# Kernel tuning notes

Measured on AMD Instinct MI355X. Metric: run time of the kernel, lower is better.

Reference implementation:

```python
import jax, jax.numpy as jnp
import numpy as np

H = 8          # num_heads
EPS = 1e-6     # layernorm epsilon
NEG_INF = -1e9


def _ln(x, g, b):
    m = jnp.mean(x, axis=-1, keepdims=True)
    v = jnp.mean(jnp.square(x - m), axis=-1, keepdims=True)
    return g * (x - m) * jax.lax.rsqrt(v + EPS) + b


def _mha(xq, kv, wq, wk, wv, wo, bias):
    # xq: [B,Tq,D], kv: [B,Tk,D]; weights [D,D]. Returns (out [B,Tq,D], weights [B,H,Tq,Tk]).
    B, Tq, D = xq.shape
    dh = D // H
    q = (xq @ wq) * (dh ** -0.5)
    k = kv @ wk
    v = kv @ wv
    q = q.reshape(B, Tq, H, dh).transpose(0, 2, 1, 3)
    k = k.reshape(B, -1, H, dh).transpose(0, 2, 1, 3)
    v = v.reshape(B, -1, H, dh).transpose(0, 2, 1, 3)
    logits = jnp.einsum('bhqd,bhkd->bhqk', q, k)
    if bias is not None:
        logits = logits + bias
    w = jax.nn.softmax(logits, axis=-1)
    out = jnp.einsum('bhqk,bhkd->bhqd', w, v).transpose(0, 2, 1, 3).reshape(B, Tq, D)
    return out @ wo, w


def setup_inputs() -> dict:
    key = jax.random.key(0)
    ks = jax.random.split(key, 16)
    B, Td, Te, D, F, L = 2, 2048, 2048, 512, 2048, 2
    s = 0.02
    inp = {
        'x': jax.random.normal(ks[0], (B, Td, D), jnp.float32),
        'enc_a': jax.random.normal(ks[1], (B, Te, D), jnp.float32),
        'enc_c': jax.random.normal(ks[2], (B, Te, D), jnp.float32),
        'sa_wq': jax.random.normal(ks[3], (L, D, D), jnp.float32) * s,
        'sa_wk': jax.random.normal(ks[4], (L, D, D), jnp.float32) * s,
        'sa_wv': jax.random.normal(ks[5], (L, D, D), jnp.float32) * s,
        'sa_wo': jax.random.normal(ks[6], (L, D, D), jnp.float32) * s,
        'ed_wq': jax.random.normal(ks[7], (L, D, D), jnp.float32) * s,
        'ed_wk': jax.random.normal(ks[8], (L, D, D), jnp.float32) * s,
        'ed_wv': jax.random.normal(ks[9], (L, D, D), jnp.float32) * s,
        'ed_wo': jax.random.normal(ks[10], (L, D, D), jnp.float32) * s,
        'ffn_w1': jax.random.normal(ks[11], (L, D, F), jnp.float32) * s,
        'ffn_w2': jax.random.normal(ks[12], (L, F, D), jnp.float32) * s,
        'ln1_g': jnp.ones((L, D), jnp.float32), 'ln1_b': jnp.zeros((L, D), jnp.float32),
        'ln2_g': jnp.ones((L, D), jnp.float32), 'ln2_b': jnp.zeros((L, D), jnp.float32),
        'ln3_g': jnp.ones((L, D), jnp.float32), 'ln3_b': jnp.zeros((L, D), jnp.float32),
        'out_g': jnp.ones((D,), jnp.float32), 'out_b': jnp.zeros((D,), jnp.float32),
    }
    return inp


def reference(x, enc_a, enc_c, sa_wq, sa_wk, sa_wv, sa_wo, ed_wq, ed_wk, ed_wv, ed_wo,
              ffn_w1, ffn_w2, ln1_g, ln1_b, ln2_g, ln2_b, ln3_g, ln3_b, out_g, out_b):
    B, T, D = x.shape
    L = sa_wq.shape[0]
    # decoder self-attention causal bias, broadcast over [B,H]
    causal = jnp.where(jnp.tril(jnp.ones((T, T), bool)), 0.0, NEG_INF)[None, None]
    avg = None
    for i in range(L):
        h = _ln(x, ln1_g[i], ln1_b[i])
        y, _ = _mha(h, h, sa_wq[i], sa_wk[i], sa_wv[i], sa_wo[i], causal)
        x = x + y  # residual (dropout inactive at eval)
        h = _ln(x, ln2_g[i], ln2_b[i])
        y0, _ = _mha(h, enc_a, ed_wq[i], ed_wk[i], ed_wv[i], ed_wo[i], None)
        y1, w = _mha(h, enc_c, ed_wq[i], ed_wk[i], ed_wv[i], ed_wo[i], None)
        # original overwrites attn_scores with second call's head-averaged weights
        scores = jnp.mean(w, axis=1) / L
        avg = scores if avg is None else avg + scores
        x = x + y0 + y1
        h = _ln(x, ln3_g[i], ln3_b[i])
        x = x + jax.nn.relu(h @ ffn_w1[i]) @ ffn_w2[i]
    x = _ln(x, out_g, out_b)
    return x, avg
```

## Files before the change

### kernel.cpp

```cpp
#include <hip/hip_runtime.h>
#include <hip/hip_bf16.h>

#define BB 2
#define TT 2048
#define DD 512
#define FF 2048
#define HH 8
#define DH 64
#define LL 2
#define MM (BB*TT)

typedef __attribute__((ext_vector_type(8))) short bf16x8;
typedef __attribute__((ext_vector_type(4))) float f32x4;

__device__ __forceinline__ float bf2f(unsigned short u) {
    return __uint_as_float(((unsigned int)u) << 16);
}
__device__ __forceinline__ unsigned short f2bf(float f) {
    unsigned int u = __float_as_uint(f);
    u += 0x7fffu + ((u >> 16) & 1u);
    return (unsigned short)(u >> 16);
}
__device__ __forceinline__ void gload16(const void* g, void* l) {
    __builtin_amdgcn_global_load_lds((__attribute__((address_space(1))) void*)g,
                                     (__attribute__((address_space(3))) void*)l, 16, 0, 0);
}

template<bool BF16OUT>
__global__ __launch_bounds__(256) void ln_kernel(const float* __restrict__ x,
                                                 const float* __restrict__ g,
                                                 const float* __restrict__ b,
                                                 void* __restrict__ out)
{
    const int row = blockIdx.x;
    const int tid = threadIdx.x;
    const float2 v = ((const float2*)(x + (size_t)row * DD))[tid];
    float s = v.x + v.y;
    float q = v.x * v.x + v.y * v.y;
    #pragma unroll
    for (int off = 32; off; off >>= 1) {
        s += __shfl_down(s, off);
        q += __shfl_down(q, off);
    }
    __shared__ float ss[4], qq[4];
    const int wid = tid >> 6;
    if ((tid & 63) == 0) { ss[wid] = s; qq[wid] = q; }
    __syncthreads();
    s = ss[0] + ss[1] + ss[2] + ss[3];
    q = qq[0] + qq[1] + qq[2] + qq[3];
    const float mean = s * (1.0f / DD);
    const float var = q * (1.0f / DD) - mean * mean;
    const float inv = rsqrtf(var + 1e-6f);
    const float2 gg = ((const float2*)g)[tid];
    const float2 bb = ((const float2*)b)[tid];
    const float ox = gg.x * (v.x - mean) * inv + bb.x;
    const float oy = gg.y * (v.y - mean) * inv + bb.y;
    if (BF16OUT) {
        const unsigned int pk = (unsigned int)f2bf(ox) | ((unsigned int)f2bf(oy) << 16);
        ((unsigned int*)((unsigned short*)out + (size_t)row * DD))[tid] = pk;
    } else {
        float2 o; o.x = ox; o.y = oy;
        ((float2*)((float*)out + (size_t)row * DD))[tid] = o;
    }
}

__global__ __launch_bounds__(256) void cvt_kernel(const float* __restrict__ src,
                                                  unsigned short* __restrict__ dst, int n)
{
    const int i = (blockIdx.x * 256 + threadIdx.x) * 8;
    if (i >= n) return;
    const float4 a = *(const float4*)(src + i);
    const float4 b = *(const float4*)(src + i + 4);
    unsigned short o[8];
    o[0] = f2bf(a.x); o[1] = f2bf(a.y); o[2] = f2bf(a.z); o[3] = f2bf(a.w);
    o[4] = f2bf(b.x); o[5] = f2bf(b.y); o[6] = f2bf(b.z); o[7] = f2bf(b.w);
    *(bf16x8*)(dst + i) = *(bf16x8*)o;
}

struct CvtJob { const float* s; unsigned short* d; };
struct CvtJobs16 { CvtJob j[16]; };

__global__ __launch_bounds__(256) void cvtT_kernel(CvtJobs16 P, int K, int N)
{
    __shared__ float t[32][33];
    const CvtJob jb = P.j[blockIdx.z];
    const int tx = threadIdx.x & 31, ty = threadIdx.x >> 5;
    const int gk = blockIdx.y << 5, gn = blockIdx.x << 5;
    #pragma unroll
    for (int i = 0; i < 4; ++i)
        t[ty + i * 8][tx] = jb.s[(size_t)(gk + ty + i * 8) * N + gn + tx];
    __syncthreads();
    #pragma unroll
    for (int i = 0; i < 4; ++i)
        jb.d[(size_t)(gn + ty + i * 8) * K + gk + tx] = f2bf(t[tx][ty + i * 8]);
}

__global__ __launch_bounds__(256) void vtrans_kernel(const unsigned short* __restrict__ v,
                                                     unsigned short* __restrict__ vt)
{
    __shared__ unsigned short tile[64][72];
    const int b = blockIdx.z, h = blockIdx.y, t0 = blockIdx.x << 6;
    const int r = threadIdx.x >> 2;
    const int s4 = threadIdx.x & 3;
    const unsigned short* src = v + (size_t)(b * TT + t0 + r) * DD + h * DH + s4 * 16;
    *(bf16x8*)&tile[r][s4 * 16] = *(const bf16x8*)src;
    *(bf16x8*)&tile[r][s4 * 16 + 8] = *(const bf16x8*)(src + 8);
    __syncthreads();
    unsigned short o[16];
    #pragma unroll
    for (int e = 0; e < 16; ++e) o[e] = tile[s4 * 16 + e][r];
    unsigned short* dst = vt + ((size_t)(b * HH + h) * DH + r) * TT + t0 + s4 * 16;
    *(bf16x8*)dst = *(bf16x8*)o;
    *(bf16x8*)(dst + 8) = *(bf16x8*)(o + 8);
}

struct GemmJob {
    const unsigned short* A;
    const unsigned short* Wt;
    const float* res;
    float* Cf;
    unsigned short* Cb;
    float scale;
    int relu;
};
struct GemmJobs6 { GemmJob j[6]; };

__global__ __launch_bounds__(256, 2) void gemm_mfma(GemmJobs6 P, int M, int N, int K)
{
    __shared__ __align__(16) unsigned char lds[32768];
    const GemmJob jb = P.j[blockIdx.z];
    const int tid = threadIdx.x, lane = tid & 63, w = tid >> 6;
    const int bn = blockIdx.x << 7, bm = blockIdx.y << 7;
    const int wr = (w >> 1) << 6, wc = (w & 1) << 6;
    const size_t strA = (size_t)K * 2;

    f32x4 acc[4][4] = {};
    const int akey = (lane & 7) << 4;
    const int frow = lane & 15;
    const int kq = (lane >> 4) << 4;

    for (int kt = 0; kt < K; kt += 64) {
        __syncthreads();
        #pragma unroll
        for (int c = 0; c < 4; ++c) {
            const int q = c * 4 + w;
            const int o = (q << 10) + (lane << 4);
            const int row = o >> 7;
            const int colb = (o & 127) ^ ((row & 7) << 4);
            gload16((const char*)jb.A + (size_t)(bm + row) * strA + kt * 2 + colb,
                    lds + (q << 10));
            gload16((const char*)jb.Wt + (size_t)(bn + row) * strA + kt * 2 + colb,
                    lds + 16384 + (q << 10));
        }
        asm volatile("s_waitcnt vmcnt(0)" ::: "memory");
        __syncthreads();
        #pragma unroll
        for (int kk = 0; kk < 2; ++kk) {
            bf16x8 av[4], bv[4];
            #pragma unroll
            for (int i = 0; i < 4; ++i) {
                const int rA = wr + (i << 4) + frow;
                av[i] = *(const bf16x8*)(lds + (rA << 7) + ((((kk << 6) + kq)) ^ akey));
                const int rB = wc + (i << 4) + frow;
                bv[i] = *(const bf16x8*)(lds + 16384 + (rB << 7) + ((((kk << 6) + kq)) ^ akey));
            }
            #pragma unroll
            for (int i = 0; i < 4; ++i)
                #pragma unroll
                for (int j = 0; j < 4; ++j)
                    acc[i][j] = __builtin_amdgcn_mfma_f32_16x16x32_bf16(av[i], bv[j], acc[i][j], 0, 0, 0);
        }
    }

    const int crow0 = (lane >> 4) << 2;
    const int ccol = lane & 15;
    #pragma unroll
    for (int i = 0; i < 4; ++i) {
        #pragma unroll
        for (int j = 0; j < 4; ++j) {
            #pragma unroll
            for (int r = 0; r < 4; ++r) {
                const int gm = bm + wr + (i << 4) + crow0 + r;
                const int gn = bn + wc + (j << 4) + ccol;
                float v = acc[i][j][r] * jb.scale;
                if (jb.relu) v = fmaxf(v, 0.f);
                const size_t idx = (size_t)gm * N + gn;
                if (jb.res) v += jb.res[idx];
                if (jb.Cf) jb.Cf[idx] = v;
                if (jb.Cb) jb.Cb[idx] = f2bf(v);
            }
        }
    }
}

template<bool CAUSAL, bool DUAL, bool STOREML>
__global__ __launch_bounds__(256, 4) void flash_mfma(
    const unsigned short* __restrict__ q,
    const unsigned short* __restrict__ ka, const unsigned short* __restrict__ vta,
    const unsigned short* __restrict__ kc, const unsigned short* __restrict__ vtc,
    unsigned short* __restrict__ outa, unsigned short* __restrict__ outc,
    float* __restrict__ ml)
{
    __shared__ __align__(16) char lds[40960];
    const int tid = threadIdx.x;
    const int lane = tid & 63, w = tid >> 6;
    const int g4 = lane >> 4, c = lane & 15;

    const int f = blockIdx.x + 32 * (blockIdx.y + 8 * blockIdx.z);
    const int xcd = f & 7;
    const int tt = f >> 3;
    const int jq = tt & 31;
    const int grp = (tt >> 5) * 8 + xcd;
    int b, h, which;
    if (DUAL) { which = grp & 1; b = (grp >> 1) & 1; h = grp >> 2; }
    else      { which = 0;       b = grp & 1;        h = grp >> 1; }
    const int q0 = jq << 6;
    const int q0w = q0 + w * 16;

    const unsigned short* k  = (DUAL && which) ? kc : ka;
    const unsigned short* vt = (DUAL && which) ? vtc : vta;
    unsigned short* out = (DUAL && which) ? outc : outa;

    bf16x8 Qf[2];
    {
        const unsigned short* qp = q + (size_t)(b * TT + q0w + c) * DD + h * DH + (g4 << 3);
        Qf[0] = *(const bf16x8*)qp;
        Qf[1] = *(const bf16x8*)(qp + 32);
    }
    const char* kbase = (const char*)(k + (size_t)b * TT * DD + h * DH);
    const char* vtb   = (const char*)(vt + (size_t)(b * HH + h) * DH * TT);
    char* Pw = lds + 32768 + w * 2048;
    const int pkey = (c & 7) << 4;

    f32x4 O[4] = {};
    float mval = -1e30f, lpart = 0.f;

    const int nt = CAUSAL ? ((q0 >> 6) + 1) : (TT >> 6);

    auto STAGE = [&](int t, int sel) {
        const int kt = t << 6;
        char* Kb = lds + sel * 8192;
        char* Vb = lds + 16384 + sel * 8192;
        #pragma unroll
        for (int c8 = 0; c8 < 2; ++c8) {
            const int qc = (c8 << 2) + w;
            const int o = (qc << 10) + (lane << 4);
            const int row = o >> 7;
            const int colb = (o & 127) ^ ((row & 7) << 4);
            gload16(kbase + (size_t)(kt + row) * (DD * 2) + colb, Kb + (qc << 10));
            gload16(vtb + (size_t)row * (TT * 2) + kt * 2 + colb, Vb + (qc << 10));
        }
    };

    STAGE(0, 0);
    asm volatile("s_waitcnt vmcnt(0)" ::: "memory");
    __syncthreads();

    for (int t = 0; t < nt; ++t) {
        const int cur = t & 1;
        if (t + 1 < nt) STAGE(t + 1, cur ^ 1);
        const char* Kb = lds + cur * 8192;
        const char* Vb = lds + 16384 + cur * 8192;

        f32x4 s[4] = {};
        #pragma unroll
        for (int kk = 0; kk < 2; ++kk) {
            bf16x8 av[4];
            #pragma unroll
            for (int i = 0; i < 4; ++i) {
                const int r = (i << 4) + c;
                av[i] = *(const bf16x8*)(Kb + (r << 7) + (((kk << 6) + (g4 << 4)) ^ ((r & 7) << 4)));
            }
            #pragma unroll
            for (int i = 0; i < 4; ++i)
                s[i] = __builtin_amdgcn_mfma_f32_16x16x32_bf16(av[i], Qf[kk], s[i], 0, 0, 0);
        }

        if (CAUSAL && t == nt - 1) {
            #pragma unroll
            for (int i = 0; i < 4; ++i)
                #pragma unroll
                for (int r = 0; r < 4; ++r)
                    if (((i << 4) + (g4 << 2) + r) > ((w << 4) + c)) s[i][r] = -1e30f;
        }

        float pmax = -1e30f;
        #pragma unroll
        for (int i = 0; i < 4; ++i)
            #pragma unroll
            for (int r = 0; r < 4; ++r) pmax = fmaxf(pmax, s[i][r]);
        if (__any(pmax > mval + 8.f)) {
            float mx = fmaxf(pmax, __shfl_xor(pmax, 16));
            mx = fmaxf(mx, __shfl_xor(mx, 32));
            const float mn = fmaxf(mval, mx);
            const float scf = __expf(mval - mn);
            lpart *= scf;
            #pragma unroll
            for (int r = 0; r < 4; ++r) {
                const float fr = __shfl(scf, (g4 << 2) + r);
                #pragma unroll
                for (int jj = 0; jj < 4; ++jj) O[jj][r] *= fr;
            }
            mval = mn;
        }
        float ps = 0.f;
        #pragma unroll
        for (int i = 0; i < 4; ++i)
            #pragma unroll
            for (int r = 0; r < 4; ++r) {
                const float p = __expf(s[i][r] - mval);
                s[i][r] = p;
                ps += p;
            }
        lpart += ps;

        #pragma unroll
        for (int i = 0; i < 4; ++i) {
            uint2 pk;
            pk.x = (unsigned int)f2bf(s[i][0]) | ((unsigned int)f2bf(s[i][1]) << 16);
            pk.y = (unsigned int)f2bf(s[i][2]) | ((unsigned int)f2bf(s[i][3]) << 16);
            const int baddr = (c << 7) + (((i << 4) + (g4 << 2)) << 1);
            *(uint2*)(Pw + (baddr ^ pkey)) = pk;
        }
        asm volatile("s_waitcnt lgkmcnt(0)" ::: "memory");
        __builtin_amdgcn_sched_barrier(0);

        #pragma unroll
        for (int kk = 0; kk < 2; ++kk) {
            const bf16x8 pa = *(const bf16x8*)(Pw + (((c << 7) + (kk << 6) + (g4 << 4)) ^ pkey));
            bf16x8 vb[4];
            #pragma unroll
            for (int jj = 0; jj < 4; ++jj) {
                const int d = (jj << 4) + c;
                vb[jj] = *(const bf16x8*)(Vb + (d << 7) + (((kk << 6) + (g4 << 4)) ^ ((d & 7) << 4)));
            }
            #pragma unroll
            for (int jj = 0; jj < 4; ++jj)
                O[jj] = __builtin_amdgcn_mfma_f32_16x16x32_bf16(pa, vb[jj], O[jj], 0, 0, 0);
        }

        asm volatile("s_waitcnt vmcnt(0)" ::: "memory");
        __syncthreads();
    }

    float l2 = lpart + __shfl_xor(lpart, 16);
    const float ltot = l2 + __shfl_xor(l2, 32);
    float invL[4];
    #pragma unroll
    for (int r = 0; r < 4; ++r) invL[r] = 1.f / __shfl(ltot, (g4 << 2) + r);
    #pragma unroll
    for (int jj = 0; jj < 4; ++jj)
        #pragma unroll
        for (int r = 0; r < 4; ++r) {
            const int qr = q0w + (g4 << 2) + r;
            out[(size_t)(b * TT + qr) * DD + h * DH + (jj << 4) + c] = f2bf(O[jj][r] * invL[r]);
        }
    if (STOREML && (!DUAL || which == 1) && lane < 16) {
        const size_t mi = (((size_t)b * HH + h) * TT + q0w + lane) * 2;
        ml[mi] = mval;
        ml[mi + 1] = ltot;
    }
}

__global__ __launch_bounds__(256) void sum_bf16_kernel(const unsigned short* __restrict__ a,
                                                       const unsigned short* __restrict__ b,
                                                       unsigned short* __restrict__ o, int n)
{
    const int i = (blockIdx.x * 256 + threadIdx.x) * 8;
    if (i >= n) return;
    const bf16x8 av = *(const bf16x8*)(a + i);
    const bf16x8 bv = *(const bf16x8*)(b + i);
    unsigned short ov[8];
    #pragma unroll
    for (int e = 0; e < 8; ++e)
        ov[e] = f2bf(bf2f(((const unsigned short*)&av)[e]) + bf2f(((const unsigned short*)&bv)[e]));
    *(bf16x8*)(o + i) = *(bf16x8*)ov;
}

__global__ __launch_bounds__(64) void avg_mfma_kernel(const unsigned short* __restrict__ qm,
                                                      const unsigned short* __restrict__ kcm,
                                                      const float* __restrict__ ml,
                                                      float* __restrict__ avg, int first)
{
    __shared__ __align__(16) unsigned char ldsQ[8192];
    __shared__ __align__(16) unsigned char ldsK[8192];
    __shared__ float sM[8][64];
    __shared__ float sIL[8][64];
    const int lane = threadIdx.x;
    const int kt0 = blockIdx.x << 6, q0 = blockIdx.y << 6, b = blockIdx.z;

    #pragma unroll
    for (int h = 0; h < 8; ++h) {
        const float* mp = ml + (((size_t)(b * HH + h) * TT) + q0 + lane) * 2;
        sM[h][lane] = mp[0];
        sIL[h][lane] = 1.f / mp[1];
    }

    float avac[4][4][4] = {};
    const int akey = (lane & 7) << 4;
    const int frow = lane & 15;
    const int kq = (lane >> 4) << 4;
    const int crow0 = (lane >> 4) << 2;

    for (int h = 0; h < 8; ++h) {
        __syncthreads();
        #pragma unroll
        for (int c = 0; c < 8; ++c) {
            const int o = (c << 10) + (lane << 4);
            const int row = o >> 7;
            const int colb = (o & 127) ^ ((row & 7) << 4);
            gload16((const char*)qm + ((size_t)(b * TT + q0 + row) * DD + h * DH) * 2 + colb,
                    ldsQ + (c << 10));
            gload16((const char*)kcm + ((size_t)(b * TT + kt0 + row) * DD + h * DH) * 2 + colb,
                    ldsK + (c << 10));
        }
        asm volatile("s_waitcnt vmcnt(0)" ::: "memory");
        __syncthreads();
        f32x4 s[4][4] = {};
        #pragma unroll
        for (int kk = 0; kk < 2; ++kk) {
            bf16x8 qv[4], kv[4];
            #pragma unroll
            for (int i = 0; i < 4; ++i) {
                qv[i] = *(const bf16x8*)(ldsQ + (((i << 4) + frow) << 7) + (((kk << 6) + kq) ^ akey));
                kv[i] = *(const bf16x8*)(ldsK + (((i << 4) + frow) << 7) + (((kk << 6) + kq) ^ akey));
            }
            #pragma unroll
            for (int i = 0; i < 4; ++i)
                #pragma unroll
                for (int j = 0; j < 4; ++j)
                    s[i][j] = __builtin_amdgcn_mfma_f32_16x16x32_bf16(qv[i], kv[j], s[i][j], 0, 0, 0);
        }
        #pragma unroll
        for (int i = 0; i < 4; ++i)
            #pragma unroll
            for (int j = 0; j < 4; ++j)
                #pragma unroll
                for (int r = 0; r < 4; ++r) {
                    const int qr = (i << 4) + crow0 + r;
                    avac[i][j][r] += __expf(s[i][j][r] - sM[h][qr]) * sIL[h][qr];
                }
    }

    float* dst = avg + ((size_t)b * TT + q0) * TT + kt0;
    #pragma unroll
    for (int i = 0; i < 4; ++i)
        #pragma unroll
        for (int j = 0; j < 4; ++j)
            #pragma unroll
            for (int r = 0; r < 4; ++r) {
                const int qr = (i << 4) + crow0 + r;
                const int kc = (j << 4) + (lane & 15);
                const float v = avac[i][j][r] * (1.f / (HH * LL));
                float* p = dst + (size_t)qr * TT + kc;
                *p = first ? v : (*p + v);
            }
}

extern "C" void kernel_launch(void* const* d_in, const int* in_sizes, int n_in,
                              void* d_out, int out_size, void* d_ws, size_t ws_size,
                              hipStream_t stream)
{
    const float* x_in   = (const float*)d_in[0];
    const float* enc_a  = (const float*)d_in[1];
    const float* enc_c  = (const float*)d_in[2];
    const float* sa_wq0 = (const float*)d_in[3];
    const float* sa_wk0 = (const float*)d_in[4];
    const float* sa_wv0 = (const float*)d_in[5];
    const float* sa_wo0 = (const float*)d_in[6];
    const float* ed_wq0 = (const float*)d_in[7];
    const float* ed_wk0 = (const float*)d_in[8];
    const float* ed_wv0 = (const float*)d_in[9];
    const float* ed_wo0 = (const float*)d_in[10];
    const float* ffn_w10 = (const float*)d_in[11];
    const float* ffn_w20 = (const float*)d_in[12];
    const float* ln1_g0 = (const float*)d_in[13];
    const float* ln1_b0 = (const float*)d_in[14];
    const float* ln2_g0 = (const float*)d_in[15];
    const float* ln2_b0 = (const float*)d_in[16];
    const float* ln3_g0 = (const float*)d_in[17];
    const float* ln3_b0 = (const float*)d_in[18];
    const float* out_g  = (const float*)d_in[19];
    const float* out_b  = (const float*)d_in[20];

    const size_t NTD = (size_t)MM * DD;
    const size_t MB = 1u << 20;
    char* W = (char*)d_ws;
    float*          x_buf   = (float*)(W);
    unsigned short* h_bf    = (unsigned short*)(W + 8 * MB);
    unsigned short* q_bf    = (unsigned short*)(W + 12 * MB);
    unsigned short* k1_bf   = (unsigned short*)(W + 16 * MB);
    unsigned short* v1_bf   = (unsigned short*)(W + 20 * MB);
    unsigned short* k2_bf   = (unsigned short*)(W + 24 * MB);
    unsigned short* v2_bf   = (unsigned short*)(W + 28 * MB);
    unsigned short* attnA   = (unsigned short*)(W + 32 * MB);
    unsigned short* attnC   = (unsigned short*)(W + 36 * MB);
    float*          ml_buf  = (float*)(W + 40 * MB);
    unsigned short* encA_bf = (unsigned short*)(W + 41 * MB);
    unsigned short* encC_bf = (unsigned short*)(W + 45 * MB);
    unsigned short* wbf     = (unsigned short*)(W + 49 * MB);
    unsigned short* ffn_bf  = q_bf;
    unsigned short* attnS   = h_bf;
    unsigned short* vt1     = h_bf;
    unsigned short* vt2     = v1_bf;

    unsigned short* w1t = wbf + (size_t)16 * DD * DD;
    unsigned short* w2t = w1t + (size_t)2 * DD * FF;
    auto wd = [&](int l, int which) { return wbf + ((size_t)(l * 8 + which)) * DD * DD; };

    float* x_out   = (float*)d_out;
    float* avg_out = (float*)d_out + NTD;

    hipMemcpyAsync(x_buf, x_in, NTD * sizeof(float), hipMemcpyDeviceToDevice, stream);

    {
        CvtJobs16 J{};
        const float* srcs[8] = {sa_wq0, sa_wk0, sa_wv0, sa_wo0, ed_wq0, ed_wk0, ed_wv0, ed_wo0};
        for (int l = 0; l < LL; ++l)
            for (int t = 0; t < 8; ++t) {
                J.j[l * 8 + t].s = srcs[t] + (size_t)l * DD * DD;
                J.j[l * 8 + t].d = wd(l, t);
            }
        cvtT_kernel<<<dim3(DD / 32, DD / 32, 16), 256, 0, stream>>>(J, DD, DD);
    }
    {
        CvtJobs16 J{};
        for (int l = 0; l < LL; ++l) { J.j[l].s = ffn_w10 + (size_t)l * DD * FF; J.j[l].d = w1t + (size_t)l * FF * DD; }
        cvtT_kernel<<<dim3(FF / 32, DD / 32, 2), 256, 0, stream>>>(J, DD, FF);
    }
    {
        CvtJobs16 J{};
        for (int l = 0; l < LL; ++l) { J.j[l].s = ffn_w20 + (size_t)l * FF * DD; J.j[l].d = w2t + (size_t)l * DD * FF; }
        cvtT_kernel<<<dim3(DD / 32, FF / 32, 2), 256, 0, stream>>>(J, FF, DD);
    }
    cvt_kernel<<<NTD / 8 / 256, 256, 0, stream>>>(enc_a, encA_bf, (int)NTD);
    cvt_kernel<<<NTD / 8 / 256, 256, 0, stream>>>(enc_c, encC_bf, (int)NTD);

    const dim3 vtG(TT / 64, HH, BB);
    const dim3 flashSelfG(TT / 64, HH, BB);
    const dim3 flashCrossG(TT / 64, HH, BB * 2);
    const dim3 avgG(TT / 64, TT / 64, BB);
    const float qscale = 0.125f;

    for (int i = 0; i < LL; ++i) {
        const size_t fOff = (size_t)i * DD * FF;
        const size_t lOff = (size_t)i * DD;

        ln_kernel<true><<<MM, 256, 0, stream>>>(x_buf, ln1_g0 + lOff, ln1_b0 + lOff, h_bf);
        {
            GemmJobs6 J{};
            J.j[0] = {h_bf, wd(i, 0), nullptr, nullptr, q_bf, qscale, 0};
            J.j[1] = {h_bf, wd(i, 1), nullptr, nullptr, k1_bf, 1.f, 0};
            J.j[2] = {h_bf, wd(i, 2), nullptr, nullptr, v1_bf, 1.f, 0};
            gemm_mfma<<<dim3(DD / 128, MM / 128, 3), 256, 0, stream>>>(J, MM, DD, DD);
        }
        vtrans_kernel<<<vtG, 256, 0, stream>>>(v1_bf, vt1);
        flash_mfma<true, false, false><<<flashSelfG, 256, 0, stream>>>(
            q_bf, k1_bf, vt1, nullptr, nullptr, attnA, nullptr, nullptr);
        {
            GemmJobs6 J{};
            J.j[0] = {attnA, wd(i, 3), x_buf, x_buf, nullptr, 1.f, 0};
            gemm_mfma<<<dim3(DD / 128, MM / 128, 1), 256, 0, stream>>>(J, MM, DD, DD);
        }

        ln_kernel<true><<<MM, 256, 0, stream>>>(x_buf, ln2_g0 + lOff, ln2_b0 + lOff, h_bf);
        {
            GemmJobs6 J{};
            J.j[0] = {h_bf,    wd(i, 4), nullptr, nullptr, q_bf, qscale, 0};
            J.j[1] = {encA_bf, wd(i, 5), nullptr, nullptr, k1_bf, 1.f, 0};
            J.j[2] = {encA_bf, wd(i, 6), nullptr, nullptr, v1_bf, 1.f, 0};
            J.j[3] = {encC_bf, wd(i, 5), nullptr, nullptr, k2_bf, 1.f, 0};
            J.j[4] = {encC_bf, wd(i, 6), nullptr, nullptr, v2_bf, 1.f, 0};
            gemm_mfma<<<dim3(DD / 128, MM / 128, 5), 256, 0, stream>>>(J, MM, DD, DD);
        }
        vtrans_kernel<<<vtG, 256, 0, stream>>>(v1_bf, vt1);
        vtrans_kernel<<<vtG, 256, 0, stream>>>(v2_bf, vt2);
        flash_mfma<false, true, true><<<flashCrossG, 256, 0, stream>>>(
            q_bf, k1_bf, vt1, k2_bf, vt2, attnA, attnC, ml_buf);
        sum_bf16_kernel<<<NTD / 8 / 256, 256, 0, stream>>>(attnA, attnC, attnS, (int)NTD);
        avg_mfma_kernel<<<avgG, 64, 0, stream>>>(q_bf, k2_bf, ml_buf, avg_out, (i == 0) ? 1 : 0);
        {
            GemmJobs6 J{};
            J.j[0] = {attnS, wd(i, 7), x_buf, x_buf, nullptr, 1.f, 0};
            gemm_mfma<<<dim3(DD / 128, MM / 128, 1), 256, 0, stream>>>(J, MM, DD, DD);
        }

        ln_kernel<true><<<MM, 256, 0, stream>>>(x_buf, ln3_g0 + lOff, ln3_b0 + lOff, h_bf);
        {
            GemmJobs6 J{};
            J.j[0] = {h_bf, w1t + fOff, nullptr, nullptr, ffn_bf, 1.f, 1};
            gemm_mfma<<<dim3(FF / 128, MM / 128, 1), 256, 0, stream>>>(J, MM, FF, DD);
        }
        {
            GemmJobs6 J{};
            J.j[0] = {ffn_bf, w2t + fOff, x_buf, x_buf, nullptr, 1.f, 0};
            gemm_mfma<<<dim3(DD / 128, MM / 128, 1), 256, 0, stream>>>(J, MM, DD, FF);
        }
    }

    ln_kernel<false><<<MM, 256, 0, stream>>>(x_buf, out_g, out_b, x_out);
}
```

Measured before the change: 653.8 us.

## Fuse V transpose into GEMM epilogue, multi-row flash tiles, exp2 softmax, packed bf16 cvt

The V projection GEMM now writes its output already transposed per head, which removes the separate vtrans kernels and their extra memory round trip. The flash kernel is templated on the number of 16-row query blocks per wave: cross-attention uses two, so each K/V tile loaded into LDS is reused for twice as many queries, and its occupancy bound is lowered to fit. Softmax switches to exp2 by folding log2(e) into the q scale, and the f32-to-bf16 conversions use the hardware packed-convert instruction. Weight and encoder conversion launches are merged into single multi-job launches, which leaves many idle early-exit blocks in the weight conversion grid.

```diff
diff --git a/kernel.cpp b/kernel.cpp
--- a/kernel.cpp
+++ b/kernel.cpp
@@ -20,6 +20,11 @@
     unsigned int u = __float_as_uint(f);
     u += 0x7fffu + ((u >> 16) & 1u);
     return (unsigned short)(u >> 16);
+}
+__device__ __forceinline__ unsigned int cvtpk(float a, float b) {
+    unsigned int r;
+    asm("v_cvt_pk_bf16_f32 %0, %1, %2" : "=v"(r) : "v"(a), "v"(b));
+    return r;
 }
 __device__ __forceinline__ void gload16(const void* g, void* l) {
     __builtin_amdgcn_global_load_lds((__attribute__((address_space(1))) void*)g,
@@ -56,7 +61,7 @@
     const float ox = gg.x * (v.x - mean) * inv + bb.x;
     const float oy = gg.y * (v.y - mean) * inv + bb.y;
     if (BF16OUT) {
-        const unsigned int pk = (unsigned int)f2bf(ox) | ((unsigned int)f2bf(oy) << 16);
+        const unsigned int pk = cvtpk(ox, oy);
         ((unsigned int*)((unsigned short*)out + (size_t)row * DD))[tid] = pk;
     } else {
         float2 o; o.x = ox; o.y = oy;
@@ -64,54 +69,39 @@
     }
 }
 
-__global__ __launch_bounds__(256) void cvt_kernel(const float* __restrict__ src,
-                                                  unsigned short* __restrict__ dst, int n)
-{
+struct CvtEJob { const float* s; unsigned short* d; };
+struct CvtEJobs2 { CvtEJob j[2]; };
+
+__global__ __launch_bounds__(256) void cvt_kernel(CvtEJobs2 P, int n)
+{
+    const CvtEJob jb = P.j[blockIdx.z];
     const int i = (blockIdx.x * 256 + threadIdx.x) * 8;
     if (i >= n) return;
-    const float4 a = *(const float4*)(src + i);
-    const float4 b = *(const float4*)(src + i + 4);
-    unsigned short o[8];
-    o[0] = f2bf(a.x); o[1] = f2bf(a.y); o[2] = f2bf(a.z); o[3] = f2bf(a.w);
-    o[4] = f2bf(b.x); o[5] = f2bf(b.y); o[6] = f2bf(b.z); o[7] = f2bf(b.w);
-    *(bf16x8*)(dst + i) = *(bf16x8*)o;
-}
-
-struct CvtJob { const float* s; unsigned short* d; };
-struct CvtJobs16 { CvtJob j[16]; };
-
-__global__ __launch_bounds__(256) void cvtT_kernel(CvtJobs16 P, int K, int N)
+    const float4 a = *(const float4*)(jb.s + i);
+    const float4 b = *(const float4*)(jb.s + i + 4);
+    unsigned int o[4];
+    o[0] = cvtpk(a.x, a.y); o[1] = cvtpk(a.z, a.w);
+    o[2] = cvtpk(b.x, b.y); o[3] = cvtpk(b.z, b.w);
+    *(bf16x8*)(jb.d + i) = *(bf16x8*)o;
+}
+
+struct CvtTJob { const float* s; unsigned short* d; int K; int N; };
+struct CvtTJobs20 { CvtTJob j[20]; };
+
+__global__ __launch_bounds__(256) void cvtT_kernel(CvtTJobs20 P)
 {
     __shared__ float t[32][33];
-    const CvtJob jb = P.j[blockIdx.z];
+    const CvtTJob jb = P.j[blockIdx.z];
+    const int gk = blockIdx.y << 5, gn = blockIdx.x << 5;
+    if (gk >= jb.K || gn >= jb.N) return;
     const int tx = threadIdx.x & 31, ty = threadIdx.x >> 5;
-    const int gk = blockIdx.y << 5, gn = blockIdx.x << 5;
     #pragma unroll
     for (int i = 0; i < 4; ++i)
-        t[ty + i * 8][tx] = jb.s[(size_t)(gk + ty + i * 8) * N + gn + tx];
+        t[ty + i * 8][tx] = jb.s[(size_t)(gk + ty + i * 8) * jb.N + gn + tx];
     __syncthreads();
     #pragma unroll
     for (int i = 0; i < 4; ++i)
-        jb.d[(size_t)(gn + ty + i * 8) * K + gk + tx] = f2bf(t[tx][ty + i * 8]);
-}
-
-__global__ __launch_bounds__(256) void vtrans_kernel(const unsigned short* __restrict__ v,
-                                                     unsigned short* __restrict__ vt)
-{
-    __shared__ unsigned short tile[64][72];
-    const int b = blockIdx.z, h = blockIdx.y, t0 = blockIdx.x << 6;
-    const int r = threadIdx.x >> 2;
-    const int s4 = threadIdx.x & 3;
-    const unsigned short* src = v + (size_t)(b * TT + t0 + r) * DD + h * DH + s4 * 16;
-    *(bf16x8*)&tile[r][s4 * 16] = *(const bf16x8*)src;
-    *(bf16x8*)&tile[r][s4 * 16 + 8] = *(const bf16x8*)(src + 8);
-    __syncthreads();
-    unsigned short o[16];
-    #pragma unroll
-    for (int e = 0; e < 16; ++e) o[e] = tile[s4 * 16 + e][r];
-    unsigned short* dst = vt + ((size_t)(b * HH + h) * DH + r) * TT + t0 + s4 * 16;
-    *(bf16x8*)dst = *(bf16x8*)o;
-    *(bf16x8*)(dst + 8) = *(bf16x8*)(o + 8);
+        jb.d[(size_t)(gn + ty + i * 8) * jb.K + gk + tx] = f2bf(t[tx][ty + i * 8]);
 }
 
 struct GemmJob {
@@ -120,6 +110,7 @@
     const float* res;
     float* Cf;
     unsigned short* Cb;
+    unsigned short* Ct;
     float scale;
     int relu;
 };
@@ -174,6 +165,22 @@
 
     const int crow0 = (lane >> 4) << 2;
     const int ccol = lane & 15;
+    if (jb.Ct) {
+        #pragma unroll
+        for (int i = 0; i < 4; ++i)
+            #pragma unroll
+            for (int j = 0; j < 4; ++j) {
+                const int gm = bm + wr + (i << 4) + crow0;
+                const int gn = bn + wc + (j << 4) + ccol;
+                const int bI = gm >> 11, t = gm & 2047;
+                const int hI = gn >> 6, d = gn & 63;
+                uint2 pk;
+                pk.x = cvtpk(acc[i][j][0], acc[i][j][1]);
+                pk.y = cvtpk(acc[i][j][2], acc[i][j][3]);
+                *(uint2*)(jb.Ct + ((size_t)((bI * HH + hI) * DH + d)) * TT + t) = pk;
+            }
+        return;
+    }
     #pragma unroll
     for (int i = 0; i < 4; ++i) {
         #pragma unroll
@@ -193,49 +200,54 @@
     }
 }
 
-template<bool CAUSAL, bool DUAL, bool STOREML>
-__global__ __launch_bounds__(256, 4) void flash_mfma(
+template<bool CAUSAL, bool DUAL, bool STOREML, int NQ>
+__global__ __launch_bounds__(256, 2) void flash_mfma(
     const unsigned short* __restrict__ q,
     const unsigned short* __restrict__ ka, const unsigned short* __restrict__ vta,
     const unsigned short* __restrict__ kc, const unsigned short* __restrict__ vtc,
     unsigned short* __restrict__ outa, unsigned short* __restrict__ outc,
     float* __restrict__ ml)
 {
-    __shared__ __align__(16) char lds[40960];
+    __shared__ __align__(16) char lds[49152];
     const int tid = threadIdx.x;
     const int lane = tid & 63, w = tid >> 6;
     const int g4 = lane >> 4, c = lane & 15;
 
-    const int f = blockIdx.x + 32 * (blockIdx.y + 8 * blockIdx.z);
+    constexpr int GX = 32 / NQ;
+    const int f = blockIdx.x + GX * (blockIdx.y + 8 * blockIdx.z);
     const int xcd = f & 7;
     const int tt = f >> 3;
-    const int jq = tt & 31;
-    const int grp = (tt >> 5) * 8 + xcd;
+    const int jq = tt % GX;
+    const int grp = (tt / GX) * 8 + xcd;
     int b, h, which;
     if (DUAL) { which = grp & 1; b = (grp >> 1) & 1; h = grp >> 2; }
     else      { which = 0;       b = grp & 1;        h = grp >> 1; }
-    const int q0 = jq << 6;
-    const int q0w = q0 + w * 16;
+    const int q0 = jq * (64 * NQ);
+    const int q0w = q0 + w * (16 * NQ);
+    const int kendw = q0w + 16 * NQ;
 
     const unsigned short* k  = (DUAL && which) ? kc : ka;
     const unsigned short* vt = (DUAL && which) ? vtc : vta;
     unsigned short* out = (DUAL && which) ? outc : outa;
 
-    bf16x8 Qf[2];
-    {
-        const unsigned short* qp = q + (size_t)(b * TT + q0w + c) * DD + h * DH + (g4 << 3);
-        Qf[0] = *(const bf16x8*)qp;
-        Qf[1] = *(const bf16x8*)(qp + 32);
+    bf16x8 Qf[NQ][2];
+    #pragma unroll
+    for (int jb = 0; jb < NQ; ++jb) {
+        const unsigned short* qp = q + (size_t)(b * TT + q0w + (jb << 4) + c) * DD + h * DH + (g4 << 3);
+        Qf[jb][0] = *(const bf16x8*)qp;
+        Qf[jb][1] = *(const bf16x8*)(qp + 32);
     }
     const char* kbase = (const char*)(k + (size_t)b * TT * DD + h * DH);
     const char* vtb   = (const char*)(vt + (size_t)(b * HH + h) * DH * TT);
-    char* Pw = lds + 32768 + w * 2048;
+    char* Pw = lds + 32768 + w * (NQ * 2048);
     const int pkey = (c & 7) << 4;
 
-    f32x4 O[4] = {};
-    float mval = -1e30f, lpart = 0.f;
-
-    const int nt = CAUSAL ? ((q0 >> 6) + 1) : (TT >> 6);
+    f32x4 O[NQ][4] = {};
+    float mval[NQ], lpart[NQ];
+    #pragma unroll
+    for (int jb = 0; jb < NQ; ++jb) { mval[jb] = -1e30f; lpart[jb] = 0.f; }
+
+    const int nt = CAUSAL ? ((q0 + 64 * NQ) >> 6) : (TT >> 6);
 
     auto STAGE = [&](int t, int sel) {
         const int kt = t << 6;
@@ -259,106 +271,119 @@
     for (int t = 0; t < nt; ++t) {
         const int cur = t & 1;
         if (t + 1 < nt) STAGE(t + 1, cur ^ 1);
-        const char* Kb = lds + cur * 8192;
-        const char* Vb = lds + 16384 + cur * 8192;
-
-        f32x4 s[4] = {};
-        #pragma unroll
-        for (int kk = 0; kk < 2; ++kk) {
-            bf16x8 av[4];
-            #pragma unroll
-            for (int i = 0; i < 4; ++i) {
-                const int r = (i << 4) + c;
-                av[i] = *(const bf16x8*)(Kb + (r << 7) + (((kk << 6) + (g4 << 4)) ^ ((r & 7) << 4)));
-            }
-            #pragma unroll
-            for (int i = 0; i < 4; ++i)
-                s[i] = __builtin_amdgcn_mfma_f32_16x16x32_bf16(av[i], Qf[kk], s[i], 0, 0, 0);
-        }
-
-        if (CAUSAL && t == nt - 1) {
-            #pragma unroll
-            for (int i = 0; i < 4; ++i)
-                #pragma unroll
-                for (int r = 0; r < 4; ++r)
-                    if (((i << 4) + (g4 << 2) + r) > ((w << 4) + c)) s[i][r] = -1e30f;
-        }
-
-        float pmax = -1e30f;
-        #pragma unroll
-        for (int i = 0; i < 4; ++i)
-            #pragma unroll
-            for (int r = 0; r < 4; ++r) pmax = fmaxf(pmax, s[i][r]);
-        if (__any(pmax > mval + 8.f)) {
-            float mx = fmaxf(pmax, __shfl_xor(pmax, 16));
-            mx = fmaxf(mx, __shfl_xor(mx, 32));
-            const float mn = fmaxf(mval, mx);
-            const float scf = __expf(mval - mn);
-            lpart *= scf;
-            #pragma unroll
-            for (int r = 0; r < 4; ++r) {
-                const float fr = __shfl(scf, (g4 << 2) + r);
-                #pragma unroll
-                for (int jj = 0; jj < 4; ++jj) O[jj][r] *= fr;
-            }
-            mval = mn;
-        }
-        float ps = 0.f;
-        #pragma unroll
-        for (int i = 0; i < 4; ++i)
-            #pragma unroll
-            for (int r = 0; r < 4; ++r) {
-                const float p = __expf(s[i][r] - mval);
-                s[i][r] = p;
-                ps += p;
-            }
-        lpart += ps;
-
-        #pragma unroll
-        for (int i = 0; i < 4; ++i) {
-            uint2 pk;
-            pk.x = (unsigned int)f2bf(s[i][0]) | ((unsigned int)f2bf(s[i][1]) << 16);
-            pk.y = (unsigned int)f2bf(s[i][2]) | ((unsigned int)f2bf(s[i][3]) << 16);
-            const int baddr = (c << 7) + (((i << 4) + (g4 << 2)) << 1);
-            *(uint2*)(Pw + (baddr ^ pkey)) = pk;
-        }
-        asm volatile("s_waitcnt lgkmcnt(0)" ::: "memory");
-        __builtin_amdgcn_sched_barrier(0);
-
-        #pragma unroll
-        for (int kk = 0; kk < 2; ++kk) {
-            const bf16x8 pa = *(const bf16x8*)(Pw + (((c << 7) + (kk << 6) + (g4 << 4)) ^ pkey));
-            bf16x8 vb[4];
-            #pragma unroll
-            for (int jj = 0; jj < 4; ++jj) {
-                const int d = (jj << 4) + c;
-                vb[jj] = *(const bf16x8*)(Vb + (d << 7) + (((kk << 6) + (g4 << 4)) ^ ((d & 7) << 4)));
-            }
-            #pragma unroll
-            for (int jj = 0; jj < 4; ++jj)
-                O[jj] = __builtin_amdgcn_mfma_f32_16x16x32_bf16(pa, vb[jj], O[jj], 0, 0, 0);
+        const int kt = t << 6;
+
+        if (!CAUSAL || kt < kendw) {
+            const char* Kb = lds + cur * 8192;
+            const char* Vb = lds + 16384 + cur * 8192;
+
+            f32x4 s[NQ][4] = {};
+            #pragma unroll
+            for (int kk = 0; kk < 2; ++kk) {
+                bf16x8 av[4];
+                #pragma unroll
+                for (int i = 0; i < 4; ++i) {
+                    const int r = (i << 4) + c;
+                    av[i] = *(const bf16x8*)(Kb + (r << 7) + (((kk << 6) + (g4 << 4)) ^ ((r & 7) << 4)));
+                }
+                #pragma unroll
+                for (int i = 0; i < 4; ++i)
+                    #pragma unroll
+                    for (int jb = 0; jb < NQ; ++jb)
+                        s[jb][i] = __builtin_amdgcn_mfma_f32_16x16x32_bf16(av[i], Qf[jb][kk], s[jb][i], 0, 0, 0);
+            }
+
+            #pragma unroll
+            for (int jb = 0; jb < NQ; ++jb) {
+                const int qbase = q0w + (jb << 4);
+                if (CAUSAL && kt + 63 > qbase) {
+                    #pragma unroll
+                    for (int i = 0; i < 4; ++i)
+                        #pragma unroll
+                        for (int r = 0; r < 4; ++r)
+                            if (kt + (i << 4) + (g4 << 2) + r > qbase + c) s[jb][i][r] = -1e30f;
+                }
+                float pmax = -1e30f;
+                #pragma unroll
+                for (int i = 0; i < 4; ++i)
+                    #pragma unroll
+                    for (int r = 0; r < 4; ++r) pmax = fmaxf(pmax, s[jb][i][r]);
+                if (__any(pmax > mval[jb] + 11.f)) {
+                    float mx = fmaxf(pmax, __shfl_xor(pmax, 16));
+                    mx = fmaxf(mx, __shfl_xor(mx, 32));
+                    const float mn = fmaxf(mval[jb], mx);
+                    const float scf = exp2f(mval[jb] - mn);
+                    lpart[jb] *= scf;
+                    #pragma unroll
+                    for (int r = 0; r < 4; ++r) {
+                        const float fr = __shfl(scf, (g4 << 2) + r);
+                        #pragma unroll
+                        for (int jj = 0; jj < 4; ++jj) O[jb][jj][r] *= fr;
+                    }
+                    mval[jb] = mn;
+                }
+                float ps = 0.f;
+                #pragma unroll
+                for (int i = 0; i < 4; ++i)
+                    #pragma unroll
+                    for (int r = 0; r < 4; ++r) {
+                        const float p = exp2f(s[jb][i][r] - mval[jb]);
+                        s[jb][i][r] = p;
+                        ps += p;
+                    }
+                lpart[jb] += ps;
+                #pragma unroll
+                for (int i = 0; i < 4; ++i) {
+                    uint2 pk;
+                    pk.x = cvtpk(s[jb][i][0], s[jb][i][1]);
+                    pk.y = cvtpk(s[jb][i][2], s[jb][i][3]);
+                    const int baddr = (((jb << 4) + c) << 7) + (((i << 4) + (g4 << 2)) << 1);
+                    *(uint2*)(Pw + (baddr ^ pkey)) = pk;
+                }
+            }
+            asm volatile("s_waitcnt lgkmcnt(0)" ::: "memory");
+            __builtin_amdgcn_sched_barrier(0);
+
+            #pragma unroll
+            for (int kk = 0; kk < 2; ++kk) {
+                bf16x8 pa[NQ];
+                #pragma unroll
+                for (int jb = 0; jb < NQ; ++jb)
+                    pa[jb] = *(const bf16x8*)(Pw + (((((jb << 4) + c) << 7) + (kk << 6) + (g4 << 4)) ^ pkey));
+                #pragma unroll
+                for (int jj = 0; jj < 4; ++jj) {
+                    const int d = (jj << 4) + c;
+                    const bf16x8 vb = *(const bf16x8*)(Vb + (d << 7) + (((kk << 6) + (g4 << 4)) ^ ((d & 7) << 4)));
+                    #pragma unroll
+                    for (int jb = 0; jb < NQ; ++jb)
+                        O[jb][jj] = __builtin_amdgcn_mfma_f32_16x16x32_bf16(pa[jb], vb, O[jb][jj], 0, 0, 0);
+                }
+            }
         }
 
         asm volatile("s_waitcnt vmcnt(0)" ::: "memory");
         __syncthreads();
     }
 
-    float l2 = lpart + __shfl_xor(lpart, 16);
-    const float ltot = l2 + __shfl_xor(l2, 32);
-    float invL[4];
-    #pragma unroll
-    for (int r = 0; r < 4; ++r) invL[r] = 1.f / __shfl(ltot, (g4 << 2) + r);
-    #pragma unroll
-    for (int jj = 0; jj < 4; ++jj)
-        #pragma unroll
-        for (int r = 0; r < 4; ++r) {
-            const int qr = q0w + (g4 << 2) + r;
-            out[(size_t)(b * TT + qr) * DD + h * DH + (jj << 4) + c] = f2bf(O[jj][r] * invL[r]);
-        }
-    if (STOREML && (!DUAL || which == 1) && lane < 16) {
-        const size_t mi = (((size_t)b * HH + h) * TT + q0w + lane) * 2;
-        ml[mi] = mval;
-        ml[mi + 1] = ltot;
+    #pragma unroll
+    for (int jb = 0; jb < NQ; ++jb) {
+        float l2 = lpart[jb] + __shfl_xor(lpart[jb], 16);
+        const float ltot = l2 + __shfl_xor(l2, 32);
+        float invL[4];
+        #pragma unroll
+        for (int r = 0; r < 4; ++r) invL[r] = 1.f / __shfl(ltot, (g4 << 2) + r);
+        #pragma unroll
+        for (int jj = 0; jj < 4; ++jj)
+            #pragma unroll
+            for (int r = 0; r < 4; ++r) {
+                const int qr = q0w + (jb << 4) + (g4 << 2) + r;
+                out[(size_t)(b * TT + qr) * DD + h * DH + (jj << 4) + c] = f2bf(O[jb][jj][r] * invL[r]);
+            }
+        if (STOREML && (!DUAL || which == 1) && lane < 16) {
+            const size_t mi = (((size_t)b * HH + h) * TT + q0w + (jb << 4) + lane) * 2;
+            ml[mi] = mval[jb];
+            ml[mi + 1] = ltot;
+        }
     }
 }
 
@@ -370,10 +395,13 @@
     if (i >= n) return;
     const bf16x8 av = *(const bf16x8*)(a + i);
     const bf16x8 bv = *(const bf16x8*)(b + i);
-    unsigned short ov[8];
-    #pragma unroll
-    for (int e = 0; e < 8; ++e)
-        ov[e] = f2bf(bf2f(((const unsigned short*)&av)[e]) + bf2f(((const unsigned short*)&bv)[e]));
+    unsigned int ov[4];
+    #pragma unroll
+    for (int e = 0; e < 4; ++e) {
+        const float lo = bf2f(((const unsigned short*)&av)[2 * e]) + bf2f(((const unsigned short*)&bv)[2 * e]);
+        const float hi = bf2f(((const unsigned short*)&av)[2 * e + 1]) + bf2f(((const unsigned short*)&bv)[2 * e + 1]);
+        ov[e] = cvtpk(lo, hi);
+    }
     *(bf16x8*)(o + i) = *(bf16x8*)ov;
 }
 
@@ -438,7 +466,7 @@
                 #pragma unroll
                 for (int r = 0; r < 4; ++r) {
                     const int qr = (i << 4) + crow0 + r;
-                    avac[i][j][r] += __expf(s[i][j][r] - sM[h][qr]) * sIL[h][qr];
+                    avac[i][j][r] += exp2f(s[i][j][r] - sM[h][qr]) * sIL[h][qr];
                 }
     }
 
@@ -490,9 +518,9 @@
     unsigned short* h_bf    = (unsigned short*)(W + 8 * MB);
     unsigned short* q_bf    = (unsigned short*)(W + 12 * MB);
     unsigned short* k1_bf   = (unsigned short*)(W + 16 * MB);
-    unsigned short* v1_bf   = (unsigned short*)(W + 20 * MB);
+    unsigned short* vt1     = (unsigned short*)(W + 20 * MB);
     unsigned short* k2_bf   = (unsigned short*)(W + 24 * MB);
-    unsigned short* v2_bf   = (unsigned short*)(W + 28 * MB);
+    unsigned short* vt2     = (unsigned short*)(W + 28 * MB);
     unsigned short* attnA   = (unsigned short*)(W + 32 * MB);
     unsigned short* attnC   = (unsigned short*)(W + 36 * MB);
     float*          ml_buf  = (float*)(W + 40 * MB);
@@ -501,8 +529,6 @@
     unsigned short* wbf     = (unsigned short*)(W + 49 * MB);
     unsigned short* ffn_bf  = q_bf;
     unsigned short* attnS   = h_bf;
-    unsigned short* vt1     = h_bf;
-    unsigned short* vt2     = v1_bf;
 
     unsigned short* w1t = wbf + (size_t)16 * DD * DD;
     unsigned short* w2t = w1t + (size_t)2 * DD * FF;
@@ -514,33 +540,28 @@
     hipMemcpyAsync(x_buf, x_in, NTD * sizeof(float), hipMemcpyDeviceToDevice, stream);
 
     {
-        CvtJobs16 J{};
+        CvtTJobs20 J{};
         const float* srcs[8] = {sa_wq0, sa_wk0, sa_wv0, sa_wo0, ed_wq0, ed_wk0, ed_wv0, ed_wo0};
         for (int l = 0; l < LL; ++l)
-            for (int t = 0; t < 8; ++t) {
-                J.j[l * 8 + t].s = srcs[t] + (size_t)l * DD * DD;
-                J.j[l * 8 + t].d = wd(l, t);
-            }
-        cvtT_kernel<<<dim3(DD / 32, DD / 32, 16), 256, 0, stream>>>(J, DD, DD);
+            for (int t = 0; t < 8; ++t)
+                J.j[l * 8 + t] = {srcs[t] + (size_t)l * DD * DD, wd(l, t), DD, DD};
+        for (int l = 0; l < LL; ++l) {
+            J.j[16 + l] = {ffn_w10 + (size_t)l * DD * FF, w1t + (size_t)l * FF * DD, DD, FF};
+            J.j[18 + l] = {ffn_w20 + (size_t)l * FF * DD, w2t + (size_t)l * DD * FF, FF, DD};
+        }
+        cvtT_kernel<<<dim3(FF / 32, FF / 32, 20), 256, 0, stream>>>(J);
     }
     {
-        CvtJobs16 J{};
-        for (int l = 0; l < LL; ++l) { J.j[l].s = ffn_w10 + (size_t)l * DD * FF; J.j[l].d = w1t + (size_t)l * FF * DD; }
-        cvtT_kernel<<<dim3(FF / 32, DD / 32, 2), 256, 0, stream>>>(J, DD, FF);
-    }
-    {
-        CvtJobs16 J{};
-        for (int l = 0; l < LL; ++l) { J.j[l].s = ffn_w20 + (size_t)l * FF * DD; J.j[l].d = w2t + (size_t)l * DD * FF; }
-        cvtT_kernel<<<dim3(DD / 32, FF / 32, 2), 256, 0, stream>>>(J, FF, DD);
-    }
-    cvt_kernel<<<NTD / 8 / 256, 256, 0, stream>>>(enc_a, encA_bf, (int)NTD);
-    cvt_kernel<<<NTD / 8 / 256, 256, 0, stream>>>(enc_c, encC_bf, (int)NTD);
-
-    const dim3 vtG(TT / 64, HH, BB);
-    const dim3 flashSelfG(TT / 64, HH, BB);
-    const dim3 flashCrossG(TT / 64, HH, BB * 2);
+        CvtEJobs2 J{};
+        J.j[0] = {enc_a, encA_bf};
+        J.j[1] = {enc_c, encC_bf};
+        cvt_kernel<<<dim3(NTD / 8 / 256, 1, 2), 256, 0, stream>>>(J, (int)NTD);
+    }
+
+    const dim3 flashSelfG(32, HH, BB);
+    const dim3 flashCrossG(16, HH, BB * 2);
     const dim3 avgG(TT / 64, TT / 64, BB);
-    const float qscale = 0.125f;
+    const float qscale = 0.125f * 1.4426950408889634f;
 
     for (int i = 0; i < LL; ++i) {
         const size_t fOff = (size_t)i * DD * FF;
@@ -549,51 +570,48 @@
         ln_kernel<true><<<MM, 256, 0, stream>>>(x_buf, ln1_g0 + lOff, ln1_b0 + lOff, h_bf);
         {
             GemmJobs6 J{};
-            J.j[0] = {h_bf, wd(i, 0), nullptr, nullptr, q_bf, qscale, 0};
-            J.j[1] = {h_bf, wd(i, 1), nullptr, nullptr, k1_bf, 1.f, 0};
-            J.j[2] = {h_bf, wd(i, 2), nullptr, nullptr, v1_bf, 1.f, 0};
+            J.j[0] = {h_bf, wd(i, 0), nullptr, nullptr, q_bf, nullptr, qscale, 0};
+            J.j[1] = {h_bf, wd(i, 1), nullptr, nullptr, k1_bf, nullptr, 1.f, 0};
+            J.j[2] = {h_bf, wd(i, 2), nullptr, nullptr, nullptr, vt1, 1.f, 0};
             gemm_mfma<<<dim3(DD / 128, MM / 128, 3), 256, 0, stream>>>(J, MM, DD, DD);
         }
-        vtrans_kernel<<<vtG, 256, 0, stream>>>(v1_bf, vt1);
-        flash_mfma<true, false, false><<<flashSelfG, 256, 0, stream>>>(
+        flash_mfma<true, false, false, 1><<<flashSelfG, 256, 0, stream>>>(
             q_bf, k1_bf, vt1, nullptr, nullptr, attnA, nullptr, nullptr);
         {
             GemmJobs6 J{};
-            J.j[0] = {attnA, wd(i, 3), x_buf, x_buf, nullptr, 1.f, 0};
+            J.j[0] = {attnA, wd(i, 3), x_buf, x_buf, nullptr, nullptr, 1.f, 0};
             gemm_mfma<<<dim3(DD / 128, MM / 128, 1), 256, 0, stream>>>(J, MM, DD, DD);
         }
 
         ln_kernel<true><<<MM, 256, 0, stream>>>(x_buf, ln2_g0 + lOff, ln2_b0 + lOff, h_bf);
         {
             GemmJobs6 J{};
-            J.j[0] = {h_bf,    wd(i, 4), nullptr, nullptr, q_bf, qscale, 0};
-            J.j[1] = {encA_bf, wd(i, 5), nullptr, nullptr, k1_bf, 1.f, 0};
-            J.j[2] = {encA_bf, wd(i, 6), nullptr, nullptr, v1_bf, 1.f, 0};
-            J.j[3] = {encC_bf, wd(i, 5), nullptr, nullptr, k2_bf, 1.f, 0};
-            J.j[4] = {encC_bf, wd(i, 6), nullptr, nullptr, v2_bf, 1.f, 0};
+            J.j[0] = {h_bf,    wd(i, 4), nullptr, nullptr, q_bf, nullptr, qscale, 0};
+            J.j[1] = {encA_bf, wd(i, 5), nullptr, nullptr, k1_bf, nullptr, 1.f, 0};
+            J.j[2] = {encA_bf, wd(i, 6), nullptr, nullptr, nullptr, vt1, 1.f, 0};
+            J.j[3] = {encC_bf, wd(i, 5), nullptr, nullptr, k2_bf, nullptr, 1.f, 0};
+            J.j[4] = {encC_bf, wd(i, 6), nullptr, nullptr, nullptr, vt2, 1.f, 0};
             gemm_mfma<<<dim3(DD / 128, MM / 128, 5), 256, 0, stream>>>(J, MM, DD, DD);
         }
-        vtrans_kernel<<<vtG, 256, 0, stream>>>(v1_bf, vt1);
-        vtrans_kernel<<<vtG, 256, 0, stream>>>(v2_bf, vt2);
-        flash_mfma<false, true, true><<<flashCrossG, 256, 0, stream>>>(
+        flash_mfma<false, true, true, 2><<<flashCrossG, 256, 0, stream>>>(
             q_bf, k1_bf, vt1, k2_bf, vt2, attnA, attnC, ml_buf);
         sum_bf16_kernel<<<NTD / 8 / 256, 256, 0, stream>>>(attnA, attnC, attnS, (int)NTD);
         avg_mfma_kernel<<<avgG, 64, 0, stream>>>(q_bf, k2_bf, ml_buf, avg_out, (i == 0) ? 1 : 0);
         {
             GemmJobs6 J{};
-            J.j[0] = {attnS, wd(i, 7), x_buf, x_buf, nullptr, 1.f, 0};
+            J.j[0] = {attnS, wd(i, 7), x_buf, x_buf, nullptr, nullptr, 1.f, 0};
             gemm_mfma<<<dim3(DD / 128, MM / 128, 1), 256, 0, stream>>>(J, MM, DD, DD);
         }
 
         ln_kernel<true><<<MM, 256, 0, stream>>>(x_buf, ln3_g0 + lOff, ln3_b0 + lOff, h_bf);
         {
             GemmJobs6 J{};
-            J.j[0] = {h_bf, w1t + fOff, nullptr, nullptr, ffn_bf, 1.f, 1};
+            J.j[0] = {h_bf, w1t + fOff, nullptr, nullptr, ffn_bf, nullptr, 1.f, 1};
             gemm_mfma<<<dim3(FF / 128, MM / 128, 1), 256, 0, stream>>>(J, MM, FF, DD);
         }
         {
             GemmJobs6 J{};
-            J.j[0] = {ffn_bf, w2t + fOff, x_buf, x_buf, nullptr, 1.f, 0};
+            J.j[0] = {ffn_bf, w2t + fOff, x_buf, x_buf, nullptr, nullptr, 1.f, 0};
             gemm_mfma<<<dim3(DD / 128, MM / 128, 1), 256, 0, stream>>>(J, MM, DD, FF);
         }
     }
```

After: 658.7 us. No clear change (+0.8%).
